# Kernel optimization log

Measured on AMD Instinct MI355X. Metric: run time of the kernel, lower is better.

The kernel has to match this reference:

```python
import jax, jax.numpy as jnp
import numpy as np


def setup_inputs() -> dict:
    key = jax.random.key(0)
    k1, k2 = jax.random.split(key)
    B, C, D = 16384, 1024, 3
    fx = jax.random.normal(k1, (B, C, D), dtype=jnp.float32)
    fy = jax.random.normal(k2, (B, C, D), dtype=jnp.float32)
    return {"fx": fx, "fy": fy}


def reference(fx, fy):
    # Cross-covariance: [B, D, D]
    H = jnp.einsum('bcd,bce->bde', fx, fy)
    # torch.svd returns (u, s, v) with H = u @ diag(s) @ v^T;
    # jnp.linalg.svd returns (u, s, vh) with H = u @ diag(s) @ vh.
    u, s, vh = jnp.linalg.svd(H, full_matrices=False)
    v = jnp.swapaxes(vh, -1, -2)
    # Kabsch rotation R = v @ u^T  -> [B, D, D]
    R = jnp.matmul(v, jnp.swapaxes(u, -1, -2))
    # Per-axis scale: norms over the points axis (dim=1) -> [B, D]
    S = jnp.linalg.norm(fy, axis=1) / jnp.linalg.norm(fx, axis=1)
    return (R, S)
```

## Files before the change

kernel.cpp:

```cpp
#include <hip/hip_runtime.h>
#include <math.h>


namespace {
constexpr int THREADS = 256;
constexpr int FLOATS_PER_BATCH = 1024 * 3;
}

__global__ __launch_bounds__(THREADS)
void align_kernel(const float* __restrict__ fx,
                  const float* __restrict__ fy,
                  float* __restrict__ out,
                  int batches)
{
    const int b = blockIdx.x;
    const int t = threadIdx.x;

    const float4* fx4 = reinterpret_cast<const float4*>(fx + (size_t)b * FLOATS_PER_BATCH);
    const float4* fy4 = reinterpret_cast<const float4*>(fy + (size_t)b * FLOATS_PER_BATCH);

    float lx[12], ly[12];
    {
        float4 a0 = fx4[3 * t + 0], a1 = fx4[3 * t + 1], a2 = fx4[3 * t + 2];
        float4 b0 = fy4[3 * t + 0], b1 = fy4[3 * t + 1], b2 = fy4[3 * t + 2];
        lx[0] = a0.x; lx[1] = a0.y; lx[2]  = a0.z; lx[3]  = a0.w;
        lx[4] = a1.x; lx[5] = a1.y; lx[6]  = a1.z; lx[7]  = a1.w;
        lx[8] = a2.x; lx[9] = a2.y; lx[10] = a2.z; lx[11] = a2.w;
        ly[0] = b0.x; ly[1] = b0.y; ly[2]  = b0.z; ly[3]  = b0.w;
        ly[4] = b1.x; ly[5] = b1.y; ly[6]  = b1.z; ly[7]  = b1.w;
        ly[8] = b2.x; ly[9] = b2.y; ly[10] = b2.z; ly[11] = b2.w;
    }

    float v[15];
#pragma unroll
    for (int i = 0; i < 15; ++i) v[i] = 0.0f;

#pragma unroll
    for (int k = 0; k < 4; ++k) {
        float px0 = lx[3 * k + 0], px1 = lx[3 * k + 1], px2 = lx[3 * k + 2];
        float py0 = ly[3 * k + 0], py1 = ly[3 * k + 1], py2 = ly[3 * k + 2];
        v[0] += px0 * py0; v[1] += px0 * py1; v[2] += px0 * py2;
        v[3] += px1 * py0; v[4] += px1 * py1; v[5] += px1 * py2;
        v[6] += px2 * py0; v[7] += px2 * py1; v[8] += px2 * py2;
        v[9]  += px0 * px0; v[10] += px1 * px1; v[11] += px2 * px2;
        v[12] += py0 * py0; v[13] += py1 * py1; v[14] += py2 * py2;
    }

#pragma unroll
    for (int i = 0; i < 15; ++i) {
#pragma unroll
        for (int s = 32; s > 0; s >>= 1) v[i] += __shfl_down(v[i], s, 64);
    }

    __shared__ float red[4][15];
    const int wave = t >> 6;
    const int lane = t & 63;
    if (lane == 0) {
#pragma unroll
        for (int i = 0; i < 15; ++i) red[wave][i] = v[i];
    }
    __syncthreads();

    if (t == 0) {
        float tot[15];
#pragma unroll
        for (int i = 0; i < 15; ++i)
            tot[i] = red[0][i] + red[1][i] + red[2][i] + red[3][i];

        double Q[9];
        double nf = 0.0;
#pragma unroll
        for (int i = 0; i < 9; ++i) { Q[i] = (double)tot[i]; nf += Q[i] * Q[i]; }
        double s0 = (nf > 0.0) ? 1.0 / sqrt(nf) : 1.0;
#pragma unroll
        for (int i = 0; i < 9; ++i) Q[i] *= s0;

        for (int it = 0; it < 9; ++it) {
            double C0 = Q[4] * Q[8] - Q[5] * Q[7];
            double C1 = Q[5] * Q[6] - Q[3] * Q[8];
            double C2 = Q[3] * Q[7] - Q[4] * Q[6];
            double C3 = Q[2] * Q[7] - Q[1] * Q[8];
            double C4 = Q[0] * Q[8] - Q[2] * Q[6];
            double C5 = Q[1] * Q[6] - Q[0] * Q[7];
            double C6 = Q[1] * Q[5] - Q[2] * Q[4];
            double C7 = Q[2] * Q[3] - Q[0] * Q[5];
            double C8 = Q[0] * Q[4] - Q[1] * Q[3];
            double det = Q[0] * C0 + Q[1] * C1 + Q[2] * C2;
            double ad = fabs(det);
            if (ad < 1e-300) { det = (det < 0.0) ? -1e-300 : 1e-300; ad = 1e-300; }
            double nq = Q[0]*Q[0]+Q[1]*Q[1]+Q[2]*Q[2]+Q[3]*Q[3]+Q[4]*Q[4]
                      + Q[5]*Q[5]+Q[6]*Q[6]+Q[7]*Q[7]+Q[8]*Q[8];
            double nc = C0*C0+C1*C1+C2*C2+C3*C3+C4*C4+C5*C5+C6*C6+C7*C7+C8*C8;
            double lam = sqrt(sqrt(nc) / (ad * sqrt(nq)));
            double hl = 0.5 * lam;
            double g  = 0.5 / (lam * det);
            double N0 = hl * Q[0] + g * C0;
            double N1 = hl * Q[1] + g * C1;
            double N2 = hl * Q[2] + g * C2;
            double N3 = hl * Q[3] + g * C3;
            double N4 = hl * Q[4] + g * C4;
            double N5 = hl * Q[5] + g * C5;
            double N6 = hl * Q[6] + g * C6;
            double N7 = hl * Q[7] + g * C7;
            double N8 = hl * Q[8] + g * C8;
            Q[0]=N0; Q[1]=N1; Q[2]=N2; Q[3]=N3; Q[4]=N4; Q[5]=N5; Q[6]=N6; Q[7]=N7; Q[8]=N8;
        }

        float* Rout = out + (size_t)b * 9;
        Rout[0] = (float)Q[0]; Rout[1] = (float)Q[3]; Rout[2] = (float)Q[6];
        Rout[3] = (float)Q[1]; Rout[4] = (float)Q[4]; Rout[5] = (float)Q[7];
        Rout[6] = (float)Q[2]; Rout[7] = (float)Q[5]; Rout[8] = (float)Q[8];

        float* Sout = out + (size_t)batches * 9 + (size_t)b * 3;
        Sout[0] = sqrtf(tot[12] / tot[9]);
        Sout[1] = sqrtf(tot[13] / tot[10]);
        Sout[2] = sqrtf(tot[14] / tot[11]);
    }
}

extern "C" void kernel_launch(void* const* d_in, const int* in_sizes, int n_in,
                              void* d_out, int out_size, void* d_ws, size_t ws_size,
                              hipStream_t stream) {
    const float* fx = (const float*)d_in[0];
    const float* fy = (const float*)d_in[1];
    float* out = (float*)d_out;
    const int batches = in_sizes[0] / FLOATS_PER_BATCH;
    align_kernel<<<batches, THREADS, 0, stream>>>(fx, fy, out, batches);
}
```

Baseline: 94.04 us.

## Split into per-wave reduction kernel and per-thread batched polar solve kernel

```diff
diff --git a/kernel.cpp b/kernel.cpp
--- a/kernel.cpp
+++ b/kernel.cpp
@@ -5,45 +5,41 @@
 namespace {
 constexpr int THREADS = 256;
 constexpr int FLOATS_PER_BATCH = 1024 * 3;
+constexpr int WS_STRIDE = 16;
 }
 
 __global__ __launch_bounds__(THREADS)
-void align_kernel(const float* __restrict__ fx,
-                  const float* __restrict__ fy,
-                  float* __restrict__ out,
-                  int batches)
+void reduce_kernel(const float* __restrict__ fx,
+                   const float* __restrict__ fy,
+                   float* __restrict__ ws)
 {
-    const int b = blockIdx.x;
-    const int t = threadIdx.x;
+    const int wave = threadIdx.x >> 6;
+    const int lane = threadIdx.x & 63;
+    const int b = blockIdx.x * 4 + wave;
 
-    const float4* fx4 = reinterpret_cast<const float4*>(fx + (size_t)b * FLOATS_PER_BATCH);
-    const float4* fy4 = reinterpret_cast<const float4*>(fy + (size_t)b * FLOATS_PER_BATCH);
-
-    float lx[12], ly[12];
-    {
-        float4 a0 = fx4[3 * t + 0], a1 = fx4[3 * t + 1], a2 = fx4[3 * t + 2];
-        float4 b0 = fy4[3 * t + 0], b1 = fy4[3 * t + 1], b2 = fy4[3 * t + 2];
-        lx[0] = a0.x; lx[1] = a0.y; lx[2]  = a0.z; lx[3]  = a0.w;
-        lx[4] = a1.x; lx[5] = a1.y; lx[6]  = a1.z; lx[7]  = a1.w;
-        lx[8] = a2.x; lx[9] = a2.y; lx[10] = a2.z; lx[11] = a2.w;
-        ly[0] = b0.x; ly[1] = b0.y; ly[2]  = b0.z; ly[3]  = b0.w;
-        ly[4] = b1.x; ly[5] = b1.y; ly[6]  = b1.z; ly[7]  = b1.w;
-        ly[8] = b2.x; ly[9] = b2.y; ly[10] = b2.z; ly[11] = b2.w;
-    }
+    const float4* fx4 = reinterpret_cast<const float4*>(fx + (size_t)b * FLOATS_PER_BATCH) + 12 * lane;
+    const float4* fy4 = reinterpret_cast<const float4*>(fy + (size_t)b * FLOATS_PER_BATCH) + 12 * lane;
 
     float v[15];
 #pragma unroll
     for (int i = 0; i < 15; ++i) v[i] = 0.0f;
 
 #pragma unroll
-    for (int k = 0; k < 4; ++k) {
-        float px0 = lx[3 * k + 0], px1 = lx[3 * k + 1], px2 = lx[3 * k + 2];
-        float py0 = ly[3 * k + 0], py1 = ly[3 * k + 1], py2 = ly[3 * k + 2];
-        v[0] += px0 * py0; v[1] += px0 * py1; v[2] += px0 * py2;
-        v[3] += px1 * py0; v[4] += px1 * py1; v[5] += px1 * py2;
-        v[6] += px2 * py0; v[7] += px2 * py1; v[8] += px2 * py2;
-        v[9]  += px0 * px0; v[10] += px1 * px1; v[11] += px2 * px2;
-        v[12] += py0 * py0; v[13] += py1 * py1; v[14] += py2 * py2;
+    for (int c = 0; c < 4; ++c) {
+        float4 a0 = fx4[3 * c + 0], a1 = fx4[3 * c + 1], a2 = fx4[3 * c + 2];
+        float4 b0 = fy4[3 * c + 0], b1 = fy4[3 * c + 1], b2 = fy4[3 * c + 2];
+        float X[12] = {a0.x, a0.y, a0.z, a0.w, a1.x, a1.y, a1.z, a1.w, a2.x, a2.y, a2.z, a2.w};
+        float Y[12] = {b0.x, b0.y, b0.z, b0.w, b1.x, b1.y, b1.z, b1.w, b2.x, b2.y, b2.z, b2.w};
+#pragma unroll
+        for (int k = 0; k < 4; ++k) {
+            float px0 = X[3 * k + 0], px1 = X[3 * k + 1], px2 = X[3 * k + 2];
+            float py0 = Y[3 * k + 0], py1 = Y[3 * k + 1], py2 = Y[3 * k + 2];
+            v[0] += px0 * py0; v[1] += px0 * py1; v[2] += px0 * py2;
+            v[3] += px1 * py0; v[4] += px1 * py1; v[5] += px1 * py2;
+            v[6] += px2 * py0; v[7] += px2 * py1; v[8] += px2 * py2;
+            v[9]  += px0 * px0; v[10] += px1 * px1; v[11] += px2 * px2;
+            v[12] += py0 * py0; v[13] += py1 * py1; v[14] += py2 * py2;
+        }
     }
 
 #pragma unroll
@@ -52,70 +48,74 @@
         for (int s = 32; s > 0; s >>= 1) v[i] += __shfl_down(v[i], s, 64);
     }
 
-    __shared__ float red[4][15];
-    const int wave = t >> 6;
-    const int lane = t & 63;
     if (lane == 0) {
+        float* w = ws + (size_t)b * WS_STRIDE;
 #pragma unroll
-        for (int i = 0; i < 15; ++i) red[wave][i] = v[i];
+        for (int i = 0; i < 15; ++i) w[i] = v[i];
     }
-    __syncthreads();
+}
 
-    if (t == 0) {
-        float tot[15];
+__global__ __launch_bounds__(THREADS)
+void solve_kernel(const float* __restrict__ ws,
+                  float* __restrict__ out,
+                  int batches)
+{
+    const int b = blockIdx.x * THREADS + threadIdx.x;
+    if (b >= batches) return;
+
+    const float4* w4 = reinterpret_cast<const float4*>(ws + (size_t)b * WS_STRIDE);
+    float4 t0 = w4[0], t1 = w4[1], t2 = w4[2], t3 = w4[3];
+    float tot[15] = {t0.x, t0.y, t0.z, t0.w, t1.x, t1.y, t1.z, t1.w,
+                     t2.x, t2.y, t2.z, t2.w, t3.x, t3.y, t3.z};
+
+    double Q[9];
+    double nf = 0.0;
 #pragma unroll
-        for (int i = 0; i < 15; ++i)
-            tot[i] = red[0][i] + red[1][i] + red[2][i] + red[3][i];
+    for (int i = 0; i < 9; ++i) { Q[i] = (double)tot[i]; nf += Q[i] * Q[i]; }
+    double s0 = (nf > 0.0) ? 1.0 / sqrt(nf) : 1.0;
+#pragma unroll
+    for (int i = 0; i < 9; ++i) Q[i] *= s0;
 
-        double Q[9];
-        double nf = 0.0;
-#pragma unroll
-        for (int i = 0; i < 9; ++i) { Q[i] = (double)tot[i]; nf += Q[i] * Q[i]; }
-        double s0 = (nf > 0.0) ? 1.0 / sqrt(nf) : 1.0;
-#pragma unroll
-        for (int i = 0; i < 9; ++i) Q[i] *= s0;
+    for (int it = 0; it < 8; ++it) {
+        double C0 = Q[4] * Q[8] - Q[5] * Q[7];
+        double C1 = Q[5] * Q[6] - Q[3] * Q[8];
+        double C2 = Q[3] * Q[7] - Q[4] * Q[6];
+        double C3 = Q[2] * Q[7] - Q[1] * Q[8];
+        double C4 = Q[0] * Q[8] - Q[2] * Q[6];
+        double C5 = Q[1] * Q[6] - Q[0] * Q[7];
+        double C6 = Q[1] * Q[5] - Q[2] * Q[4];
+        double C7 = Q[2] * Q[3] - Q[0] * Q[5];
+        double C8 = Q[0] * Q[4] - Q[1] * Q[3];
+        double det = Q[0] * C0 + Q[1] * C1 + Q[2] * C2;
+        double ad = fabs(det);
+        if (ad < 1e-300) { det = (det < 0.0) ? -1e-300 : 1e-300; ad = 1e-300; }
+        double nq = Q[0]*Q[0]+Q[1]*Q[1]+Q[2]*Q[2]+Q[3]*Q[3]+Q[4]*Q[4]
+                  + Q[5]*Q[5]+Q[6]*Q[6]+Q[7]*Q[7]+Q[8]*Q[8];
+        double nc = C0*C0+C1*C1+C2*C2+C3*C3+C4*C4+C5*C5+C6*C6+C7*C7+C8*C8;
+        double lam = sqrt(sqrt(nc) / (ad * sqrt(nq)));
+        double hl = 0.5 * lam;
+        double g  = 0.5 / (lam * det);
+        double N0 = hl * Q[0] + g * C0;
+        double N1 = hl * Q[1] + g * C1;
+        double N2 = hl * Q[2] + g * C2;
+        double N3 = hl * Q[3] + g * C3;
+        double N4 = hl * Q[4] + g * C4;
+        double N5 = hl * Q[5] + g * C5;
+        double N6 = hl * Q[6] + g * C6;
+        double N7 = hl * Q[7] + g * C7;
+        double N8 = hl * Q[8] + g * C8;
+        Q[0]=N0; Q[1]=N1; Q[2]=N2; Q[3]=N3; Q[4]=N4; Q[5]=N5; Q[6]=N6; Q[7]=N7; Q[8]=N8;
+    }
 
-        for (int it = 0; it < 9; ++it) {
-            double C0 = Q[4] * Q[8] - Q[5] * Q[7];
-            double C1 = Q[5] * Q[6] - Q[3] * Q[8];
-            double C2 = Q[3] * Q[7] - Q[4] * Q[6];
-            double C3 = Q[2] * Q[7] - Q[1] * Q[8];
-            double C4 = Q[0] * Q[8] - Q[2] * Q[6];
-            double C5 = Q[1] * Q[6] - Q[0] * Q[7];
-            double C6 = Q[1] * Q[5] - Q[2] * Q[4];
-            double C7 = Q[2] * Q[3] - Q[0] * Q[5];
-            double C8 = Q[0] * Q[4] - Q[1] * Q[3];
-            double det = Q[0] * C0 + Q[1] * C1 + Q[2] * C2;
-            double ad = fabs(det);
-            if (ad < 1e-300) { det = (det < 0.0) ? -1e-300 : 1e-300; ad = 1e-300; }
-            double nq = Q[0]*Q[0]+Q[1]*Q[1]+Q[2]*Q[2]+Q[3]*Q[3]+Q[4]*Q[4]
-                      + Q[5]*Q[5]+Q[6]*Q[6]+Q[7]*Q[7]+Q[8]*Q[8];
-            double nc = C0*C0+C1*C1+C2*C2+C3*C3+C4*C4+C5*C5+C6*C6+C7*C7+C8*C8;
-            double lam = sqrt(sqrt(nc) / (ad * sqrt(nq)));
-            double hl = 0.5 * lam;
-            double g  = 0.5 / (lam * det);
-            double N0 = hl * Q[0] + g * C0;
-            double N1 = hl * Q[1] + g * C1;
-            double N2 = hl * Q[2] + g * C2;
-            double N3 = hl * Q[3] + g * C3;
-            double N4 = hl * Q[4] + g * C4;
-            double N5 = hl * Q[5] + g * C5;
-            double N6 = hl * Q[6] + g * C6;
-            double N7 = hl * Q[7] + g * C7;
-            double N8 = hl * Q[8] + g * C8;
-            Q[0]=N0; Q[1]=N1; Q[2]=N2; Q[3]=N3; Q[4]=N4; Q[5]=N5; Q[6]=N6; Q[7]=N7; Q[8]=N8;
-        }
+    float* Rout = out + (size_t)b * 9;
+    Rout[0] = (float)Q[0]; Rout[1] = (float)Q[3]; Rout[2] = (float)Q[6];
+    Rout[3] = (float)Q[1]; Rout[4] = (float)Q[4]; Rout[5] = (float)Q[7];
+    Rout[6] = (float)Q[2]; Rout[7] = (float)Q[5]; Rout[8] = (float)Q[8];
 
-        float* Rout = out + (size_t)b * 9;
-        Rout[0] = (float)Q[0]; Rout[1] = (float)Q[3]; Rout[2] = (float)Q[6];
-        Rout[3] = (float)Q[1]; Rout[4] = (float)Q[4]; Rout[5] = (float)Q[7];
-        Rout[6] = (float)Q[2]; Rout[7] = (float)Q[5]; Rout[8] = (float)Q[8];
-
-        float* Sout = out + (size_t)batches * 9 + (size_t)b * 3;
-        Sout[0] = sqrtf(tot[12] / tot[9]);
-        Sout[1] = sqrtf(tot[13] / tot[10]);
-        Sout[2] = sqrtf(tot[14] / tot[11]);
-    }
+    float* Sout = out + (size_t)batches * 9 + (size_t)b * 3;
+    Sout[0] = sqrtf(tot[12] / tot[9]);
+    Sout[1] = sqrtf(tot[13] / tot[10]);
+    Sout[2] = sqrtf(tot[14] / tot[11]);
 }
 
 extern "C" void kernel_launch(void* const* d_in, const int* in_sizes, int n_in,
@@ -124,6 +124,9 @@
     const float* fx = (const float*)d_in[0];
     const float* fy = (const float*)d_in[1];
     float* out = (float*)d_out;
+    float* ws = (float*)d_ws;
     const int batches = in_sizes[0] / FLOATS_PER_BATCH;
-    align_kernel<<<batches, THREADS, 0, stream>>>(fx, fy, out, batches);
+
+    reduce_kernel<<<batches / 4, THREADS, 0, stream>>>(fx, fy, ws);
+    solve_kernel<<<(batches + THREADS - 1) / THREADS, THREADS, 0, stream>>>(ws, out, batches);
 }
```

Measured after the change: 116.5 us. +23.9%, slower.
